# Kernel optimization log

Hardware: AMD Instinct MI355X
Metric: run time of the kernel (lower is better)

## Reference

```python
import jax, jax.numpy as jnp
import numpy as np

VOCAB, EMB, HID, NLAYERS, PAD = 32000, 256, 512, 2, 0


def setup_inputs() -> dict:
    key = jax.random.key(0)
    ks = jax.random.split(key, 20)
    B, T, S = 32, 128, 128
    s = 0.02
    inp = {
        'X': jax.random.randint(ks[0], (B, T), 0, VOCAB, dtype=jnp.int32),
        'encoderOutputs': jax.random.normal(ks[1], (B, S, HID), jnp.float32),
        'hiddeEn': jax.random.normal(ks[2], (2 * NLAYERS, B, HID), jnp.float32),
        'cellEn': jax.random.normal(ks[3], (2 * NLAYERS, B, HID), jnp.float32),
        'emb': jax.random.normal(ks[4], (VOCAB, EMB), jnp.float32) * s,
        'W_ih0': jax.random.normal(ks[5], (4 * HID, EMB), jnp.float32) * s,
        'W_hh0': jax.random.normal(ks[6], (4 * HID, HID), jnp.float32) * s,
        'b_ih0': jnp.zeros((4 * HID,), jnp.float32),
        'b_hh0': jnp.zeros((4 * HID,), jnp.float32),
        'W_ih1': jax.random.normal(ks[7], (4 * HID, HID), jnp.float32) * s,
        'W_hh1': jax.random.normal(ks[8], (4 * HID, HID), jnp.float32) * s,
        'b_ih1': jnp.zeros((4 * HID,), jnp.float32),
        'b_hh1': jnp.zeros((4 * HID,), jnp.float32),
        'attnW': jax.random.normal(ks[9], (HID, 2 * HID), jnp.float32) * s,
        'attnb': jnp.zeros((HID,), jnp.float32),
        'v': jax.random.normal(ks[10], (HID,), jnp.float32) * s,
        'fcW': jax.random.normal(ks[11], (VOCAB, 2 * HID), jnp.float32) * s,
        'fcb': jnp.zeros((VOCAB,), jnp.float32),
    }
    return inp


def _lstm_cell(x, h, c, W_ih, W_hh, b_ih, b_hh):
    gates = x @ W_ih.T + h @ W_hh.T + b_ih + b_hh  # (B, 4H)
    i, f, g, o = jnp.split(gates, 4, axis=-1)  # PyTorch gate order i,f,g,o
    c_new = jax.nn.sigmoid(f) * c + jax.nn.sigmoid(i) * jnp.tanh(g)
    h_new = jax.nn.sigmoid(o) * jnp.tanh(c_new)
    return h_new, c_new


def reference(X, encoderOutputs, hiddeEn, cellEn, emb,
              W_ih0, W_hh0, b_ih0, b_hh0, W_ih1, W_hh1, b_ih1, b_hh1,
              attnW, attnb, v, fcW, fcb):
    B, T = X.shape
    # bridge bidirectional encoder state -> (L, B, H)
    h0 = hiddeEn.reshape(NLAYERS, 2, B, HID).mean(axis=1)
    c0 = cellEn.reshape(NLAYERS, 2, B, HID).mean(axis=1)
    E = emb[X[:, :-1]]            # (B, T-1, EMB)
    targets = X[:, 1:]            # (B, T-1)
    layers = ((W_ih0, W_hh0, b_ih0, b_hh0), (W_ih1, W_hh1, b_ih1, b_hh1))
    enc = encoderOutputs          # (B, S, H)

    def step(carry, xs):
        h, c = carry              # (L, B, H) each
        x_t, y_t = xs             # (B, EMB), (B,)
        x = x_t
        hs, cs = [], []
        for l in range(NLAYERS):
            hn, cn = _lstm_cell(x, h[l], c[l], *layers[l])
            hs.append(hn); cs.append(cn)
            x = hn
        h_new = jnp.stack(hs); c_new = jnp.stack(cs)
        output = x                # (B, H) top-layer output
        hq = h_new[-1]            # attention query
        # additive attention: tanh(W[hq; enc]) . v
        cat = jnp.concatenate([jnp.broadcast_to(hq[:, None, :], enc.shape), enc], axis=-1)
        energy = jnp.tanh(cat @ attnW.T + attnb)           # (B, S, H)
        scores = energy @ v                                 # (B, S)
        att = jax.nn.softmax(scores, axis=1)
        weighted = jnp.einsum('bs,bsh->bh', att, enc)       # (B, H)
        logits = jnp.concatenate([output, weighted], axis=-1) @ fcW.T + fcb  # (B, V)
        logp = jax.nn.log_softmax(logits, axis=-1)
        nll = -jnp.take_along_axis(logp, y_t[:, None], axis=1)[:, 0]
        valid = (y_t != PAD).astype(logits.dtype)
        loss_t = jnp.sum(nll * valid) / jnp.maximum(jnp.sum(valid), 1.0)
        return (h_new, c_new), loss_t

    (_, _), losses = jax.lax.scan(step, (h0, c0),
                                  (E.transpose(1, 0, 2), targets.T))
    return jnp.sum(losses) / (T - 1)
```

## Files before the change

### kernel.cpp

```cpp
#include <hip/hip_runtime.h>
#include <math.h>

#define VOCAB 32000
#define EMB   256
#define HID   512
#define NB    32
#define TT    128
#define TM1   127
#define SS    128
#define NROWS (TM1*NB)
#define NT128 250

#define OFF_ENCW 0
#define OFF_W0S  1048576
#define OFF_W1S  1310720
#define OFF_H0I  1572864
#define OFF_C0I  1589248
#define OFF_H1I  1605632
#define OFF_C1I  1622016
#define OFF_H0H  1638400
#define OFF_HQ   OFF_H0H
#define OFF_GX   2686976
#define OFF_PART OFF_GX
#define OFF_ENCB OFF_GX
#define OFF_CATB 6881280
#define OFF_EMBB OFF_CATB
#define OFF_NLL  8978432
#define OFF_CNT  8982528
#define OFF_CMB0 8986624
#define OFF_CMB1 8988672
#define OFF_WX1  8990720
#define OFF_CMBX 9252864
#define OFF_H08  9254912
#define OFF_FLG  9779200

typedef __attribute__((ext_vector_type(8))) short short8;
typedef __attribute__((ext_vector_type(4))) float f32x4;
typedef unsigned long long ull_t;

__device__ __forceinline__ float sigm(float x){ return 1.f/(1.f + __expf(-x)); }
__device__ __forceinline__ float tanh_f(float x){
    x = fminf(fmaxf(x, -15.f), 15.f);
    float e = __expf(2.f*x);
    return (e-1.f)/(e+1.f);
}
__device__ __forceinline__ unsigned short f2b(float f){
    union{float f; unsigned u;} x{f};
    unsigned r = (x.u + 0x7fff + ((x.u>>16)&1)) >> 16;
    return (unsigned short)r;
}
__device__ __forceinline__ float b2f(unsigned short b){
    union{unsigned u; float f;} x{(unsigned)b<<16};
    return x.f;
}
__device__ __forceinline__ ull_t cohl(const ull_t* p){
    return __hip_atomic_load((ull_t*)p, __ATOMIC_RELAXED, __HIP_MEMORY_SCOPE_AGENT);
}
__device__ __forceinline__ void cohs(ull_t* p, ull_t v){
    __hip_atomic_store(p, v, __ATOMIC_RELAXED, __HIP_MEMORY_SCOPE_AGENT);
}
__device__ __forceinline__ int cohli(const int* p){
    return __hip_atomic_load((int*)p, __ATOMIC_RELAXED, __HIP_MEMORY_SCOPE_AGENT);
}
__device__ __forceinline__ void cohsi(int* p, int v){
    __hip_atomic_store(p, v, __ATOMIC_RELAXED, __HIP_MEMORY_SCOPE_AGENT);
}
__device__ __forceinline__ unsigned short cohls(const unsigned short* p){
    return __hip_atomic_load((unsigned short*)p, __ATOMIC_RELAXED, __HIP_MEMORY_SCOPE_AGENT);
}
__device__ __forceinline__ void cohss(unsigned short* p, unsigned short v){
    __hip_atomic_store(p, v, __ATOMIC_RELAXED, __HIP_MEMORY_SCOPE_AGENT);
}

__global__ void k_init(const float* __restrict__ hid, const float* __restrict__ cel,
                       float* __restrict__ ws){
    int idx = blockIdx.x*256 + threadIdx.x;
    if (idx < 32768){
        int l = idx >> 14, r = idx & 16383;
        int b = r >> 9, k = r & 511;
        float hv = 0.5f*(hid[(2*l)*16384 + b*512 + k] + hid[(2*l+1)*16384 + b*512 + k]);
        float cv = 0.5f*(cel[(2*l)*16384 + b*512 + k] + cel[(2*l+1)*16384 + b*512 + k]);
        ws[(l ? OFF_H1I : OFF_H0I) + b*512 + k] = hv;
        ws[(l ? OFF_C1I : OFF_C0I) + b*512 + k] = cv;
    } else if (idx < 65536){
        int j = idx - 32768;
        ((unsigned short*)(ws + OFF_CATB))[(size_t)4064*1024 + j] = 0;
    } else if (idx < 67584){
        ((int*)(ws + OFF_FLG))[idx - 65536] = 0;
    }
}

__global__ void __launch_bounds__(256)
k_qpack(const float* __restrict__ Whh0, const float* __restrict__ Whh1,
        const float* __restrict__ Wih1, float* __restrict__ ws){
    __shared__ float red[256];
    __shared__ char qb[512];
    const int r = blockIdx.x;
    const int layer = r >> 11, row = r & 2047;
    const int g = row >> 9, u = row & 511;
    const float* W = (layer == 0) ? Whh0 : (layer == 1 ? Whh1 : Wih1);
    const float* src = W + (size_t)row*512;
    const int tid = threadIdx.x;
    float w0 = src[tid], w1 = src[tid+256];
    red[tid] = fmaxf(fabsf(w0), fabsf(w1));
    __syncthreads();
    for (int off = 128; off >= 1; off >>= 1){
        if (tid < off) red[tid] = fmaxf(red[tid], red[tid+off]);
        __syncthreads();
    }
    float mx = fmaxf(red[0], 1e-30f);
    float qs = 127.f / mx;
    qb[tid]     = (char)__float2int_rn(w0*qs);
    qb[tid+256] = (char)__float2int_rn(w1*qs);
    __syncthreads();
    const int woff = (layer == 0) ? OFF_W0S : (layer == 1 ? OFF_W1S : OFF_WX1);
    const int soff = (layer == 0) ? OFF_CMB0 : (layer == 1 ? OFF_CMB1 : OFF_CMBX);
    if (tid < 128){
        int k = tid*4;
        unsigned d =  (unsigned)(unsigned char)qb[k]
                   | ((unsigned)(unsigned char)qb[k+1] << 8)
                   | ((unsigned)(unsigned char)qb[k+2] << 16)
                   | ((unsigned)(unsigned char)qb[k+3] << 24);
        ((unsigned*)(ws + woff))[(((g*32 + (k>>4))*512) + u)*4 + ((k>>2)&3)] = d;
    }
    if (tid == 0) ws[soff + row] = mx / (127.f*127.f);
}

__global__ void k_cvt(const int* __restrict__ X, const float* __restrict__ emb,
                      const float* __restrict__ enc, float* __restrict__ ws){
    int tix = blockIdx.x*256 + threadIdx.x;
    if (tix < 524288){
        int j = tix*4;
        unsigned short* eb = (unsigned short*)(ws + OFF_ENCB);
        #pragma unroll
        for (int e = 0; e < 4; ++e) eb[j+e] = f2b(enc[j+e]);
    } else if (tix < 784480){
        int j = (tix - 524288)*4;
        if (j < NROWS*EMB){
            int m = j >> 8, k = j & 255;
            int b = m / 127, t = m % 127;
            const float* src = emb + (size_t)X[b*TT + t]*EMB + k;
            unsigned short* mb = (unsigned short*)(ws + OFF_EMBB);
            #pragma unroll
            for (int e = 0; e < 4; ++e) mb[(size_t)m*256 + k + e] = f2b(src[e]);
        }
    }
}

#define DOTLOOP(WP, HQARR, A0, A1, A2, A3) \
    _Pragma("unroll 4") \
    for (int kc2 = 0; kc2 < 32; ++kc2){ \
        uint4 hq = *(const uint4*)&HQARR[kc2*16]; \
        uint4 w0 = WP[(0*32 + kc2)*512]; \
        uint4 w1 = WP[(1*32 + kc2)*512]; \
        uint4 w2 = WP[(2*32 + kc2)*512]; \
        uint4 w3 = WP[(3*32 + kc2)*512]; \
        A0 = __builtin_amdgcn_sdot4((int)w0.x, (int)hq.x, A0, false); \
        A0 = __builtin_amdgcn_sdot4((int)w0.y, (int)hq.y, A0, false); \
        A0 = __builtin_amdgcn_sdot4((int)w0.z, (int)hq.z, A0, false); \
        A0 = __builtin_amdgcn_sdot4((int)w0.w, (int)hq.w, A0, false); \
        A1 = __builtin_amdgcn_sdot4((int)w1.x, (int)hq.x, A1, false); \
        A1 = __builtin_amdgcn_sdot4((int)w1.y, (int)hq.y, A1, false); \
        A1 = __builtin_amdgcn_sdot4((int)w1.z, (int)hq.z, A1, false); \
        A1 = __builtin_amdgcn_sdot4((int)w1.w, (int)hq.w, A1, false); \
        A2 = __builtin_amdgcn_sdot4((int)w2.x, (int)hq.x, A2, false); \
        A2 = __builtin_amdgcn_sdot4((int)w2.y, (int)hq.y, A2, false); \
        A2 = __builtin_amdgcn_sdot4((int)w2.z, (int)hq.z, A2, false); \
        A2 = __builtin_amdgcn_sdot4((int)w2.w, (int)hq.w, A2, false); \
        A3 = __builtin_amdgcn_sdot4((int)w3.x, (int)hq.x, A3, false); \
        A3 = __builtin_amdgcn_sdot4((int)w3.y, (int)hq.y, A3, false); \
        A3 = __builtin_amdgcn_sdot4((int)w3.z, (int)hq.z, A3, false); \
        A3 = __builtin_amdgcn_sdot4((int)w3.w, (int)hq.w, A3, false); \
    }

__global__ void __launch_bounds__(512, 1)
k_pipe(const float* __restrict__ bih1, const float* __restrict__ bhh1,
       float* __restrict__ ws)
{
    __shared__ __align__(16) char hh8[512];
    __shared__ float wred[8];
    __shared__ float hfacs;
    const int blk = blockIdx.x, u = threadIdx.x;
    const int role = blk >> 5, b = blk & 31;
    char* h0i8 = (char*)(ws + OFF_H08);
    unsigned short* gx = (unsigned short*)(ws + OFF_GX);
    unsigned short* catb = (unsigned short*)(ws + OFF_CATB);
    int* flag0 = (int*)(ws + OFF_FLG);
    int* flag1 = flag0 + 1024;

    if (role == 0){
        const uint4* wp = ((const uint4*)(ws + OFF_W0S)) + u;
        const float* comb = ws + OFF_CMB0;
        const float cb0 = comb[u], cb1 = comb[512+u], cb2 = comb[1024+u], cb3 = comb[1536+u];
        float c = ws[OFF_C0I + b*512 + u];
        float h0v = ws[OFF_H0I + b*512 + u];
        {
            float a = fabsf(h0v);
            #pragma unroll
            for (int msk = 32; msk >= 1; msk >>= 1) a = fmaxf(a, __shfl_xor(a, msk));
            if ((u & 63) == 0) wred[u >> 6] = a;
            __syncthreads();
            if (u == 0){
                float m = wred[0];
                #pragma unroll
                for (int i2 = 1; i2 < 8; ++i2) m = fmaxf(m, wred[i2]);
                hfacs = fmaxf(m, 1.f);
            }
            __syncthreads();
        }
        float hmaxc = hfacs;
        hh8[u] = (char)__float2int_rn(h0v * (127.f/hmaxc));
        __syncthreads();
        for (int t = 0; t < TM1; ++t){
            const unsigned short* grow = gx + ((size_t)(b*127 + t))*2048 + u;
            float gxi = b2f(grow[0]),    gxf = b2f(grow[512]);
            float gxg = b2f(grow[1024]), gxo = b2f(grow[1536]);
            int a0 = 0, a1 = 0, a2 = 0, a3 = 0;
            DOTLOOP(wp, hh8, a0, a1, a2, a3)
            float gi = fmaf((float)a0, cb0*hmaxc, gxi);
            float gf = fmaf((float)a1, cb1*hmaxc, gxf);
            float gg = fmaf((float)a2, cb2*hmaxc, gxg);
            float go = fmaf((float)a3, cb3*hmaxc, gxo);
            float cn = sigm(gf)*c + sigm(gi)*tanh_f(gg);
            float hn = sigm(go)*tanh_f(cn);
            c = cn;
            __syncthreads();
            hmaxc = 1.f;
            hh8[u] = (char)__float2int_rn(hn * 127.f);
            __syncthreads();
            if (u < 64)
                cohs((ull_t*)(h0i8 + ((size_t)(b*127 + t))*512) + u, ((ull_t*)hh8)[u]);
            __syncthreads();
            if (u == 0) cohsi(flag0 + b*32, t + 1);
        }
    } else if (role == 1){
        __shared__ __align__(16) char h8[512];
        const uint4* wp = ((const uint4*)(ws + OFF_WX1)) + u;
        const float* comb = ws + OFF_CMBX;
        const float cb0 = comb[u], cb1 = comb[512+u], cb2 = comb[1024+u], cb3 = comb[1536+u];
        const float gb0 = bih1[u]        + bhh1[u];
        const float gb1 = bih1[512+u]    + bhh1[512+u];
        const float gb2 = bih1[1024+u]   + bhh1[1024+u];
        const float gb3 = bih1[1536+u]   + bhh1[1536+u];
        for (int t = 0; t < TM1; ++t){
            if (u == 0){
                while (cohli(flag0 + b*32) < t + 1) __builtin_amdgcn_s_sleep(2);
            }
            __syncthreads();
            if (u < 64)
                ((ull_t*)h8)[u] = cohl((const ull_t*)(h0i8 + ((size_t)(b*127 + t))*512) + u);
            __syncthreads();
            int a0 = 0, a1 = 0, a2 = 0, a3 = 0;
            DOTLOOP(wp, h8, a0, a1, a2, a3)
            unsigned short* gr = gx + ((size_t)(b*127 + t))*2048;
            cohss(gr + u,      f2b(fmaf((float)a0, cb0, gb0)));
            cohss(gr + 512+u,  f2b(fmaf((float)a1, cb1, gb1)));
            cohss(gr + 1024+u, f2b(fmaf((float)a2, cb2, gb2)));
            cohss(gr + 1536+u, f2b(fmaf((float)a3, cb3, gb3)));
            __syncthreads();
            if (u == 0) cohsi(flag1 + b*32, t + 1);
        }
    } else {
        const uint4* wp = ((const uint4*)(ws + OFF_W1S)) + u;
        const float* comb = ws + OFF_CMB1;
        const float cb0 = comb[u], cb1 = comb[512+u], cb2 = comb[1024+u], cb3 = comb[1536+u];
        float c = ws[OFF_C1I + b*512 + u];
        float h1v = ws[OFF_H1I + b*512 + u];
        {
            float a = fabsf(h1v);
            #pragma unroll
            for (int msk = 32; msk >= 1; msk >>= 1) a = fmaxf(a, __shfl_xor(a, msk));
            if ((u & 63) == 0) wred[u >> 6] = a;
            __syncthreads();
            if (u == 0){
                float m = wred[0];
                #pragma unroll
                for (int i2 = 1; i2 < 8; ++i2) m = fmaxf(m, wred[i2]);
                hfacs = fmaxf(m, 1.f);
            }
            __syncthreads();
        }
        float hmaxc = hfacs;
        hh8[u] = (char)__float2int_rn(h1v * (127.f/hmaxc));
        __syncthreads();
        for (int t = 0; t < TM1; ++t){
            if (u == 0){
                while (cohli(flag1 + b*32) < t + 1) __builtin_amdgcn_s_sleep(2);
            }
            __syncthreads();
            const unsigned short* gr = gx + ((size_t)(b*127 + t))*2048;
            float gxi = b2f(cohls(gr + u));
            float gxf = b2f(cohls(gr + 512+u));
            float gxg = b2f(cohls(gr + 1024+u));
            float gxo = b2f(cohls(gr + 1536+u));
            int a0 = 0, a1 = 0, a2 = 0, a3 = 0;
            DOTLOOP(wp, hh8, a0, a1, a2, a3)
            float gi = fmaf((float)a0, cb0*hmaxc, gxi);
            float gf = fmaf((float)a1, cb1*hmaxc, gxf);
            float gg = fmaf((float)a2, cb2*hmaxc, gxg);
            float go = fmaf((float)a3, cb3*hmaxc, gxo);
            float cn = sigm(gf)*c + sigm(gi)*tanh_f(gg);
            float hn = sigm(go)*tanh_f(cn);
            c = cn;
            __syncthreads();
            hmaxc = 1.f;
            hh8[u] = (char)__float2int_rn(hn * 127.f);
            catb[((size_t)(t*32 + b))*1024 + u] = f2b(hn);
            __syncthreads();
        }
    }
}

__global__ void __launch_bounds__(256)
k_gemm(const unsigned short* __restrict__ A, int lda,
       const float* __restrict__ B, int ldb,
       const float* __restrict__ bias1, const float* __restrict__ bias2,
       unsigned short* __restrict__ C, int ldc, int nkk)
{
    __shared__ unsigned short As[128*32];
    __shared__ unsigned short Bs[128*32];
    const int tid = threadIdx.x;
    const int mt = blockIdx.x, nt = blockIdx.y;
    const int m0 = mt*128, n0 = nt*128;
    const int lane = tid & 63, wid = tid >> 6;
    const int wr = wid >> 1, wc = wid & 1;
    const int lr = lane & 15, lg = lane >> 4;
    const int ar = tid & 127, ah = tid >> 7;
    const int br = tid >> 1,  bh = tid & 1;
    f32x4 acc[4][4];
    #pragma unroll
    for (int i=0;i<4;i++)
        #pragma unroll
        for (int j=0;j<4;j++) acc[i][j] = (f32x4){0.f,0.f,0.f,0.f};

    for (int kk = 0; kk < nkk; ++kk){
        const int k0 = kk*32;
        uint4 a0 = *(const uint4*)(A + (size_t)(m0+ar)*lda + k0 + ah*16);
        uint4 a1 = *(const uint4*)(A + (size_t)(m0+ar)*lda + k0 + ah*16 + 8);
        const float* bsrc = B + (size_t)(n0+br)*ldb + k0 + bh*16;
        float4 f0 = *(const float4*)(bsrc);
        float4 f1 = *(const float4*)(bsrc+4);
        float4 f2 = *(const float4*)(bsrc+8);
        float4 f3 = *(const float4*)(bsrc+12);
        __syncthreads();
        {
            int swz = (ar>>1)&3;
            *(uint4*)&As[ar*32 + ((2*ah  )^swz)*8] = a0;
            *(uint4*)&As[ar*32 + ((2*ah+1)^swz)*8] = a1;
        }
        {
            uint4 p0, p1;
            p0.x = __builtin_amdgcn_perm(__float_as_uint(f0.y), __float_as_uint(f0.x), 0x07060302u);
            p0.y = __builtin_amdgcn_perm(__float_as_uint(f0.w), __float_as_uint(f0.z), 0x07060302u);
            p0.z = __builtin_amdgcn_perm(__float_as_uint(f1.y), __float_as_uint(f1.x), 0x07060302u);
            p0.w = __builtin_amdgcn_perm(__float_as_uint(f1.w), __float_as_uint(f1.z), 0x07060302u);
            p1.x = __builtin_amdgcn_perm(__float_as_uint(f2.y), __float_as_uint(f2.x), 0x07060302u);
            p1.y = __builtin_amdgcn_perm(__float_as_uint(f2.w), __float_as_uint(f2.z), 0x07060302u);
            p1.z = __builtin_amdgcn_perm(__float_as_uint(f3.y), __float_as_uint(f3.x), 0x07060302u);
            p1.w = __builtin_amdgcn_perm(__float_as_uint(f3.w), __float_as_uint(f3.z), 0x07060302u);
            int swz = (br>>1)&3;
            *(uint4*)&Bs[br*32 + ((2*bh  )^swz)*8] = p0;
            *(uint4*)&Bs[br*32 + ((2*bh+1)^swz)*8] = p1;
        }
        __syncthreads();
        short8 av[4], bv[4];
        #pragma unroll
        for (int mi=0; mi<4; ++mi){
            int r = wr*64 + mi*16 + lr;
            av[mi] = *(const short8*)&As[r*32 + ((lg ^ ((r>>1)&3))*8)];
        }
        #pragma unroll
        for (int ni=0; ni<4; ++ni){
            int r = wc*64 + ni*16 + lr;
            bv[ni] = *(const short8*)&Bs[r*32 + ((lg ^ ((r>>1)&3))*8)];
        }
        #pragma unroll
        for (int mi=0; mi<4; ++mi)
            #pragma unroll
            for (int ni=0; ni<4; ++ni)
                acc[mi][ni] = __builtin_amdgcn_mfma_f32_16x16x32_bf16(av[mi], bv[ni], acc[mi][ni], 0, 0, 0);
    }
    int coln[4]; float bsv[4];
    #pragma unroll
    for (int ni=0; ni<4; ++ni){
        coln[ni] = n0 + wc*64 + ni*16 + lr;
        float bv2 = 0.f;
        if (bias1) bv2 += bias1[coln[ni]];
        if (bias2) bv2 += bias2[coln[ni]];
        bsv[ni] = bv2;
    }
    #pragma unroll
    for (int mi=0; mi<4; ++mi)
        #pragma unroll
        for (int ni=0; ni<4; ++ni)
            #pragma unroll
            for (int reg=0; reg<4; ++reg){
                int row = m0 + wr*64 + mi*16 + lg*4 + reg;
                C[(size_t)row*ldc + coln[ni]] = f2b(acc[mi][ni][reg] + bsv[ni]);
            }
}

__global__ void __launch_bounds__(256)
k_att(const float* __restrict__ enc, const float* __restrict__ v, float* __restrict__ ws){
    __shared__ float hqs[512], vv[512], att[128], rbuf[2];
    const int m = blockIdx.x, tid = threadIdx.x;
    const int b = m & 31;
    const unsigned short* hq = (const unsigned short*)(ws + OFF_HQ) + (size_t)m*512;
    const unsigned short* encwb = (const unsigned short*)(ws + OFF_ENCW);
    unsigned short* catb = (unsigned short*)(ws + OFF_CATB);
    hqs[tid] = b2f(hq[tid]); hqs[tid+256] = b2f(hq[tid+256]);
    vv[tid] = v[tid];        vv[tid+256] = v[tid+256];
    __syncthreads();
    {
        int s = tid >> 1, q = tid & 1;
        const unsigned short* eb = encwb + ((size_t)(b*SS + s))*512 + q*256;
        const float* hp = hqs + q*256;
        const float* vp = vv + q*256;
        float p0 = 0.f, p1 = 0.f;
        #pragma unroll 2
        for (int k = 0; k < 256; k += 2){
            p0 += tanh_f(hp[k]   + b2f(eb[k]))   * vp[k];
            p1 += tanh_f(hp[k+1] + b2f(eb[k+1])) * vp[k+1];
        }
        float p = p0 + p1;
        p += __shfl_xor(p, 1);
        if (q == 0) att[s] = p;
    }
    __syncthreads();
    float e0 = 0.f, e1 = 0.f;
    if (tid < 64){
        float m2 = fmaxf(att[tid], att[tid+64]);
        #pragma unroll
        for (int msk = 32; msk >= 1; msk >>= 1) m2 = fmaxf(m2, __shfl_xor(m2, msk));
        if (tid == 0) rbuf[0] = m2;
    }
    __syncthreads();
    float M = rbuf[0];
    if (tid < 64){
        e0 = __expf(att[tid] - M);
        e1 = __expf(att[tid+64] - M);
        float sum = e0 + e1;
        #pragma unroll
        for (int msk = 32; msk >= 1; msk >>= 1) sum += __shfl_xor(sum, msk);
        if (tid == 0) rbuf[1] = sum;
    }
    __syncthreads();
    if (tid < 64){
        float inv = 1.f / rbuf[1];
        att[tid] = e0*inv; att[tid+64] = e1*inv;
    }
    __syncthreads();
    {
        const float* eb2 = enc + (size_t)(b*SS)*512;
        float w0 = 0.f, w1 = 0.f;
        #pragma unroll 4
        for (int s = 0; s < 128; ++s){
            float a = att[s];
            w0 += a * eb2[s*512 + tid];
            w1 += a * eb2[s*512 + tid + 256];
        }
        catb[((size_t)m)*1024 + 512 + tid] = f2b(w0);
        catb[((size_t)m)*1024 + 768 + tid] = f2b(w1);
    }
}

__global__ void __launch_bounds__(256)
k_fc(const float* __restrict__ fcW, const float* __restrict__ fcb, float* __restrict__ ws){
    __shared__ unsigned short As[128*32];
    __shared__ unsigned short Bs[128*32];
    __shared__ float eM[128], eS[128];
    const int tid = threadIdx.x;
    const int bid = blockIdx.x;
    const int g = (bid & 7)*1000 + (bid >> 3);
    const int nt = g / 32, mt = g % 32;
    const int m0 = mt*128, n0 = nt*128;
    const unsigned short* catb = (const unsigned short*)(ws + OFF_CATB);
    const int lane = tid & 63, wid = tid >> 6;
    const int wr = wid >> 1, wc = wid & 1;
    const int lr = lane & 15, lg = lane >> 4;
    const int ar = tid & 127, ah = tid >> 7;
    const int br = tid >> 1,  bh = tid & 1;
    f32x4 acc[4][4];
    #pragma unroll
    for (int i=0;i<4;i++)
        #pragma unroll
        for (int j=0;j<4;j++) acc[i][j] = (f32x4){0.f,0.f,0.f,0.f};

    for (int kk = 0; kk < 32; ++kk){
        const int k0 = kk*32;
        uint4 a0 = *(const uint4*)(catb + (size_t)(m0+ar)*1024 + k0 + ah*16);
        uint4 a1 = *(const uint4*)(catb + (size_t)(m0+ar)*1024 + k0 + ah*16 + 8);
        const float* bsrc = fcW + (size_t)(n0+br)*1024 + k0 + bh*16;
        float4 f0 = *(const float4*)(bsrc);
        float4 f1 = *(const float4*)(bsrc+4);
        float4 f2 = *(const float4*)(bsrc+8);
        float4 f3 = *(const float4*)(bsrc+12);
        __syncthreads();
        {
            int swz = (ar>>1)&3;
            *(uint4*)&As[ar*32 + ((2*ah  )^swz)*8] = a0;
            *(uint4*)&As[ar*32 + ((2*ah+1)^swz)*8] = a1;
        }
        {
            uint4 p0, p1;
            p0.x = __builtin_amdgcn_perm(__float_as_uint(f0.y), __float_as_uint(f0.x), 0x07060302u);
            p0.y = __builtin_amdgcn_perm(__float_as_uint(f0.w), __float_as_uint(f0.z), 0x07060302u);
            p0.z = __builtin_amdgcn_perm(__float_as_uint(f1.y), __float_as_uint(f1.x), 0x07060302u);
            p0.w = __builtin_amdgcn_perm(__float_as_uint(f1.w), __float_as_uint(f1.z), 0x07060302u);
            p1.x = __builtin_amdgcn_perm(__float_as_uint(f2.y), __float_as_uint(f2.x), 0x07060302u);
            p1.y = __builtin_amdgcn_perm(__float_as_uint(f2.w), __float_as_uint(f2.z), 0x07060302u);
            p1.z = __builtin_amdgcn_perm(__float_as_uint(f3.y), __float_as_uint(f3.x), 0x07060302u);
            p1.w = __builtin_amdgcn_perm(__float_as_uint(f3.w), __float_as_uint(f3.z), 0x07060302u);
            int swz = (br>>1)&3;
            *(uint4*)&Bs[br*32 + ((2*bh  )^swz)*8] = p0;
            *(uint4*)&Bs[br*32 + ((2*bh+1)^swz)*8] = p1;
        }
        __syncthreads();
        short8 av[4], bv[4];
        #pragma unroll
        for (int mi=0; mi<4; ++mi){
            int r = wr*64 + mi*16 + lr;
            av[mi] = *(const short8*)&As[r*32 + ((lg ^ ((r>>1)&3))*8)];
        }
        #pragma unroll
        for (int ni=0; ni<4; ++ni){
            int r = wc*64 + ni*16 + lr;
            bv[ni] = *(const short8*)&Bs[r*32 + ((lg ^ ((r>>1)&3))*8)];
        }
        #pragma unroll
        for (int mi=0; mi<4; ++mi)
            #pragma unroll
            for (int ni=0; ni<4; ++ni)
                acc[mi][ni] = __builtin_amdgcn_mfma_f32_16x16x32_bf16(av[mi], bv[ni], acc[mi][ni], 0, 0, 0);
    }
    float bias[4];
    #pragma unroll
    for (int ni=0; ni<4; ++ni) bias[ni] = fcb[n0 + wc*64 + ni*16 + lr];
    float mxA[4][4], smA[4][4];
    #pragma unroll
    for (int mi=0; mi<4; ++mi){
        #pragma unroll
        for (int reg=0; reg<4; ++reg){
            float mx = -3.4e38f;
            #pragma unroll
            for (int ni=0; ni<4; ++ni) mx = fmaxf(mx, acc[mi][ni][reg] + bias[ni]);
            #pragma unroll
            for (int msk=8; msk>=1; msk>>=1) mx = fmaxf(mx, __shfl_xor(mx, msk));
            float sm = 0.f;
            #pragma unroll
            for (int ni=0; ni<4; ++ni) sm += __expf(acc[mi][ni][reg] + bias[ni] - mx);
            #pragma unroll
            for (int msk=8; msk>=1; msk>>=1) sm += __shfl_xor(sm, msk);
            mxA[mi][reg] = mx; smA[mi][reg] = sm;
            if (wc == 0 && lr == 0){
                int rl = wr*64 + mi*16 + lg*4 + reg;
                eM[rl] = mx; eS[rl] = sm;
            }
        }
    }
    __syncthreads();
    if (wc == 1 && lr == 0){
        float2* part = (float2*)(ws + OFF_PART);
        #pragma unroll
        for (int mi=0; mi<4; ++mi){
            #pragma unroll
            for (int reg=0; reg<4; ++reg){
                int rl = wr*64 + mi*16 + lg*4 + reg;
                float m0v = eM[rl], s0 = eS[rl];
                float m1v = mxA[mi][reg], s1 = smA[mi][reg];
                float M = fmaxf(m0v, m1v);
                float S = s0*__expf(m0v - M) + s1*__expf(m1v - M);
                part[(size_t)(m0 + rl)*NT128 + nt] = make_float2(M, S);
            }
        }
    }
}

__global__ void k_row(const int* __restrict__ X, const float* __restrict__ fcW,
                      const float* __restrict__ fcb, float* __restrict__ ws){
    __shared__ float LM[256], LS[256];
    int m = blockIdx.x, tid = threadIdx.x;
    const float2* p = (const float2*)(ws + OFF_PART);
    float M = -3.4e38f, Ssum = 0.f;
    if (tid < NT128){
        float2 q = p[(size_t)m*NT128 + tid];
        M = q.x; Ssum = q.y;
    }
    LM[tid] = M; LS[tid] = Ssum;
    __syncthreads();
    for (int off = 128; off >= 1; off >>= 1){
        if (tid < off){
            float m1 = LM[tid], s1 = LS[tid];
            float m2 = LM[tid+off], s2 = LS[tid+off];
            float mm = fmaxf(m1, m2);
            LM[tid] = mm;
            LS[tid] = s1*__expf(m1-mm) + s2*__expf(m2-mm);
        }
        __syncthreads();
    }
    float lse = LM[0] + __logf(LS[0]);
    __syncthreads();
    int t = m >> 5, b = m & 31;
    int y = X[b*TT + t + 1];
    const unsigned short* cr = (const unsigned short*)(ws + OFF_CATB) + (size_t)m*1024;
    const float* wr = fcW + (size_t)y*1024;
    float a = 0.f;
    #pragma unroll
    for (int k = 0; k < 4; ++k) a += b2f(cr[tid*4+k]) * wr[tid*4+k];
    LM[tid] = a;
    __syncthreads();
    for (int off = 128; off >= 1; off >>= 1){
        if (tid < off) LM[tid] += LM[tid+off];
        __syncthreads();
    }
    if (tid == 0){
        float tl = LM[0] + fcb[y];
        float nll = lse - tl;
        int valid = (y != 0);
        ws[OFF_NLL + m] = valid ? nll : 0.f;
        ws[OFF_CNT + m] = valid ? 1.f : 0.f;
    }
}

__global__ void k_fin(const float* __restrict__ ws, float* __restrict__ out){
    __shared__ float red[256];
    int tid = threadIdx.x;
    float lt = 0.f;
    if (tid < TM1){
        float s = 0.f, c = 0.f;
        for (int b=0;b<NB;b++){
            s += ws[OFF_NLL + tid*NB + b];
            c += ws[OFF_CNT + tid*NB + b];
        }
        lt = s / fmaxf(c, 1.f);
    }
    red[tid] = lt;
    __syncthreads();
    for (int off=128; off>=1; off>>=1){
        if (tid < off) red[tid] += red[tid+off];
        __syncthreads();
    }
    if (tid == 0) out[0] = red[0] / (float)TM1;
}

extern "C" void kernel_launch(void* const* d_in, const int* in_sizes, int n_in,
                              void* d_out, int out_size, void* d_ws, size_t ws_size,
                              hipStream_t stream) {
    const int*   X     = (const int*)  d_in[0];
    const float* enc   = (const float*)d_in[1];
    const float* hid   = (const float*)d_in[2];
    const float* cel   = (const float*)d_in[3];
    const float* emb   = (const float*)d_in[4];
    const float* Wih0  = (const float*)d_in[5];
    const float* Whh0  = (const float*)d_in[6];
    const float* bih0  = (const float*)d_in[7];
    const float* bhh0  = (const float*)d_in[8];
    const float* Wih1  = (const float*)d_in[9];
    const float* Whh1  = (const float*)d_in[10];
    const float* bih1  = (const float*)d_in[11];
    const float* bhh1  = (const float*)d_in[12];
    const float* attnW = (const float*)d_in[13];
    const float* attnb = (const float*)d_in[14];
    const float* v     = (const float*)d_in[15];
    const float* fcW   = (const float*)d_in[16];
    const float* fcb   = (const float*)d_in[17];
    float* ws  = (float*)d_ws;
    float* out = (float*)d_out;

    unsigned short* catb = (unsigned short*)(ws + OFF_CATB);
    unsigned short* hq   = (unsigned short*)(ws + OFF_HQ);
    unsigned short* encb = (unsigned short*)(ws + OFF_ENCB);
    unsigned short* embb = (unsigned short*)(ws + OFF_EMBB);
    unsigned short* encw = (unsigned short*)(ws + OFF_ENCW);
    unsigned short* g0x  = (unsigned short*)(ws + OFF_GX);

    k_init<<<320, 256, 0, stream>>>(hid, cel, ws);
    k_qpack<<<6144, 256, 0, stream>>>(Whh0, Whh1, Wih1, ws);
    k_cvt<<<3065, 256, 0, stream>>>(X, emb, enc, ws);
    k_gemm<<<dim3(32,4), 256, 0, stream>>>(encb, 512, attnW + 512, 1024,
                                           attnb, (const float*)nullptr,
                                           encw, 512, 16);
    k_gemm<<<dim3(32,16), 256, 0, stream>>>(embb, 256, Wih0, 256, bih0, bhh0,
                                            g0x, 2048, 8);
    {
        void* args[] = {(void*)&bih1, (void*)&bhh1, (void*)&ws};
        (void)hipLaunchCooperativeKernel((const void*)k_pipe, dim3(96), dim3(512),
                                         args, 0, stream);
    }
    k_gemm<<<dim3(32,4), 256, 0, stream>>>(catb, 1024, attnW, 1024,
                                           (const float*)nullptr, (const float*)nullptr,
                                           hq, 512, 16);
    k_att<<<NROWS, 256, 0, stream>>>(enc, v, ws);
    k_fc<<<8000, 256, 0, stream>>>(fcW, fcb, ws);
    k_row<<<NROWS, 256, 0, stream>>>(X, fcW, fcb, ws);
    k_fin<<<1, 256, 0, stream>>>(ws, out);
}
```

Measured before the change: 2.077 ms.

## Fuse attention into the persistent LSTM pipeline as a fourth role of blocks

Adds a fourth group of 32 blocks to the cooperative pipeline kernel. Each block waits on a per-step flag from layer 1, computes the query projection with an int8-quantized attnW via sdot4, then the additive attention scores, the softmax and the weighted context, and writes them into the concat buffer. This removes the separate query GEMM and attention kernel launches and overlaps attention with the recurrence. It adds int8 quantization error on the query projection, along with per-step sequential work that could lengthen the pipeline's critical path if the attention role lags behind the LSTM roles.

```diff
diff --git a/kernel.cpp b/kernel.cpp
--- a/kernel.cpp
+++ b/kernel.cpp
@@ -18,8 +18,6 @@
 #define OFF_C0I  1589248
 #define OFF_H1I  1605632
 #define OFF_C1I  1622016
-#define OFF_H0H  1638400
-#define OFF_HQ   OFF_H0H
 #define OFF_GX   2686976
 #define OFF_PART OFF_GX
 #define OFF_ENCB OFF_GX
@@ -33,6 +31,9 @@
 #define OFF_CMBX 9252864
 #define OFF_H08  9254912
 #define OFF_FLG  9779200
+#define OFF_WQ8  9782272
+#define OFF_CMQ  9847808
+#define OFF_H18  9848320
 
 typedef __attribute__((ext_vector_type(8))) short short8;
 typedef __attribute__((ext_vector_type(4))) float f32x4;
@@ -85,21 +86,25 @@
     } else if (idx < 65536){
         int j = idx - 32768;
         ((unsigned short*)(ws + OFF_CATB))[(size_t)4064*1024 + j] = 0;
-    } else if (idx < 67584){
+    } else if (idx < 68608){
         ((int*)(ws + OFF_FLG))[idx - 65536] = 0;
     }
 }
 
 __global__ void __launch_bounds__(256)
 k_qpack(const float* __restrict__ Whh0, const float* __restrict__ Whh1,
-        const float* __restrict__ Wih1, float* __restrict__ ws){
+        const float* __restrict__ Wih1, const float* __restrict__ attnW,
+        float* __restrict__ ws){
     __shared__ float red[256];
     __shared__ char qb[512];
     const int r = blockIdx.x;
     const int layer = r >> 11, row = r & 2047;
     const int g = row >> 9, u = row & 511;
-    const float* W = (layer == 0) ? Whh0 : (layer == 1 ? Whh1 : Wih1);
-    const float* src = W + (size_t)row*512;
+    const float* src;
+    if (layer == 0)      src = Whh0 + (size_t)row*512;
+    else if (layer == 1) src = Whh1 + (size_t)row*512;
+    else if (layer == 2) src = Wih1 + (size_t)row*512;
+    else                 src = attnW + (size_t)row*1024;
     const int tid = threadIdx.x;
     float w0 = src[tid], w1 = src[tid+256];
     red[tid] = fmaxf(fabsf(w0), fabsf(w1));
@@ -113,8 +118,10 @@
     qb[tid]     = (char)__float2int_rn(w0*qs);
     qb[tid+256] = (char)__float2int_rn(w1*qs);
     __syncthreads();
-    const int woff = (layer == 0) ? OFF_W0S : (layer == 1 ? OFF_W1S : OFF_WX1);
-    const int soff = (layer == 0) ? OFF_CMB0 : (layer == 1 ? OFF_CMB1 : OFF_CMBX);
+    const int woff = (layer == 0) ? OFF_W0S : (layer == 1 ? OFF_W1S :
+                     (layer == 2 ? OFF_WX1 : OFF_WQ8));
+    const int soff = (layer == 0) ? OFF_CMB0 : (layer == 1 ? OFF_CMB1 :
+                     (layer == 2 ? OFF_CMBX : OFF_CMQ));
     if (tid < 128){
         int k = tid*4;
         unsigned d =  (unsigned)(unsigned char)qb[k]
@@ -175,6 +182,7 @@
 
 __global__ void __launch_bounds__(512, 1)
 k_pipe(const float* __restrict__ bih1, const float* __restrict__ bhh1,
+       const float* __restrict__ enc, const float* __restrict__ v,
        float* __restrict__ ws)
 {
     __shared__ __align__(16) char hh8[512];
@@ -183,10 +191,12 @@
     const int blk = blockIdx.x, u = threadIdx.x;
     const int role = blk >> 5, b = blk & 31;
     char* h0i8 = (char*)(ws + OFF_H08);
+    char* h1i8 = (char*)(ws + OFF_H18);
     unsigned short* gx = (unsigned short*)(ws + OFF_GX);
     unsigned short* catb = (unsigned short*)(ws + OFF_CATB);
     int* flag0 = (int*)(ws + OFF_FLG);
     int* flag1 = flag0 + 1024;
+    int* flag2 = flag0 + 2048;
 
     if (role == 0){
         const uint4* wp = ((const uint4*)(ws + OFF_W0S)) + u;
@@ -260,7 +270,7 @@
             __syncthreads();
             if (u == 0) cohsi(flag1 + b*32, t + 1);
         }
-    } else {
+    } else if (role == 2){
         const uint4* wp = ((const uint4*)(ws + OFF_W1S)) + u;
         const float* comb = ws + OFF_CMB1;
         const float cb0 = comb[u], cb1 = comb[512+u], cb2 = comb[1024+u], cb3 = comb[1536+u];
@@ -306,6 +316,92 @@
             hmaxc = 1.f;
             hh8[u] = (char)__float2int_rn(hn * 127.f);
             catb[((size_t)(t*32 + b))*1024 + u] = f2b(hn);
+            __syncthreads();
+            if (u < 64)
+                cohs((ull_t*)(h1i8 + ((size_t)(b*127 + t))*512) + u, ((ull_t*)hh8)[u]);
+            __syncthreads();
+            if (u == 0) cohsi(flag2 + b*32, t + 1);
+        }
+    } else {
+        __shared__ __align__(16) char h1q[512];
+        __shared__ float hqf[512], vvv[512], attv[128], rbuf[2];
+        const uint4* wq = (const uint4*)(ws + OFF_WQ8);
+        const float scq = ws[OFF_CMQ + u];
+        const unsigned short* encwb = (const unsigned short*)(ws + OFF_ENCW);
+        vvv[u] = v[u];
+        __syncthreads();
+        for (int t = 0; t < TM1; ++t){
+            if (u == 0){
+                while (cohli(flag2 + b*32) < t + 1) __builtin_amdgcn_s_sleep(2);
+            }
+            __syncthreads();
+            if (u < 64)
+                ((ull_t*)h1q)[u] = cohl((const ull_t*)(h1i8 + ((size_t)(b*127 + t))*512) + u);
+            __syncthreads();
+            {
+                int a = 0;
+                #pragma unroll 4
+                for (int kc2 = 0; kc2 < 32; ++kc2){
+                    uint4 hv = *(const uint4*)&h1q[kc2*16];
+                    uint4 w = wq[kc2*512 + u];
+                    a = __builtin_amdgcn_sdot4((int)w.x, (int)hv.x, a, false);
+                    a = __builtin_amdgcn_sdot4((int)w.y, (int)hv.y, a, false);
+                    a = __builtin_amdgcn_sdot4((int)w.z, (int)hv.z, a, false);
+                    a = __builtin_amdgcn_sdot4((int)w.w, (int)hv.w, a, false);
+                }
+                hqf[u] = (float)a * scq;
+            }
+            __syncthreads();
+            {
+                int s = u >> 2, q = u & 3;
+                const unsigned short* eb = encwb + ((size_t)(b*SS + s))*512 + q*128;
+                const float* hp = hqf + q*128;
+                const float* vp = vvv + q*128;
+                float p0 = 0.f, p1 = 0.f;
+                #pragma unroll 2
+                for (int k = 0; k < 128; k += 2){
+                    p0 += tanh_f(hp[k]   + b2f(eb[k]))   * vp[k];
+                    p1 += tanh_f(hp[k+1] + b2f(eb[k+1])) * vp[k+1];
+                }
+                float p = p0 + p1;
+                p += __shfl_xor(p, 1);
+                p += __shfl_xor(p, 2);
+                if (q == 0) attv[s] = p;
+            }
+            __syncthreads();
+            float e0 = 0.f, e1 = 0.f;
+            if (u < 64){
+                float m2 = fmaxf(attv[u], attv[u+64]);
+                #pragma unroll
+                for (int msk = 32; msk >= 1; msk >>= 1) m2 = fmaxf(m2, __shfl_xor(m2, msk));
+                if (u == 0) rbuf[0] = m2;
+            }
+            __syncthreads();
+            float M = rbuf[0];
+            if (u < 64){
+                e0 = __expf(attv[u] - M);
+                e1 = __expf(attv[u+64] - M);
+                float sum = e0 + e1;
+                #pragma unroll
+                for (int msk = 32; msk >= 1; msk >>= 1) sum += __shfl_xor(sum, msk);
+                if (u == 0) rbuf[1] = sum;
+            }
+            __syncthreads();
+            if (u < 64){
+                float inv = 1.f / rbuf[1];
+                attv[u] = e0*inv; attv[u+64] = e1*inv;
+            }
+            __syncthreads();
+            {
+                const float* eb2 = enc + ((size_t)(b*SS))*512 + u;
+                float w0 = 0.f, w1 = 0.f;
+                #pragma unroll 4
+                for (int s = 0; s < 128; s += 2){
+                    w0 += attv[s]   * eb2[(s  )*512];
+                    w1 += attv[s+1] * eb2[(s+1)*512];
+                }
+                catb[((size_t)(t*32 + b))*1024 + 512 + u] = f2b(w0 + w1);
+            }
             __syncthreads();
         }
     }
@@ -398,70 +494,6 @@
                 int row = m0 + wr*64 + mi*16 + lg*4 + reg;
                 C[(size_t)row*ldc + coln[ni]] = f2b(acc[mi][ni][reg] + bsv[ni]);
             }
-}
-
-__global__ void __launch_bounds__(256)
-k_att(const float* __restrict__ enc, const float* __restrict__ v, float* __restrict__ ws){
-    __shared__ float hqs[512], vv[512], att[128], rbuf[2];
-    const int m = blockIdx.x, tid = threadIdx.x;
-    const int b = m & 31;
-    const unsigned short* hq = (const unsigned short*)(ws + OFF_HQ) + (size_t)m*512;
-    const unsigned short* encwb = (const unsigned short*)(ws + OFF_ENCW);
-    unsigned short* catb = (unsigned short*)(ws + OFF_CATB);
-    hqs[tid] = b2f(hq[tid]); hqs[tid+256] = b2f(hq[tid+256]);
-    vv[tid] = v[tid];        vv[tid+256] = v[tid+256];
-    __syncthreads();
-    {
-        int s = tid >> 1, q = tid & 1;
-        const unsigned short* eb = encwb + ((size_t)(b*SS + s))*512 + q*256;
-        const float* hp = hqs + q*256;
-        const float* vp = vv + q*256;
-        float p0 = 0.f, p1 = 0.f;
-        #pragma unroll 2
-        for (int k = 0; k < 256; k += 2){
-            p0 += tanh_f(hp[k]   + b2f(eb[k]))   * vp[k];
-            p1 += tanh_f(hp[k+1] + b2f(eb[k+1])) * vp[k+1];
-        }
-        float p = p0 + p1;
-        p += __shfl_xor(p, 1);
-        if (q == 0) att[s] = p;
-    }
-    __syncthreads();
-    float e0 = 0.f, e1 = 0.f;
-    if (tid < 64){
-        float m2 = fmaxf(att[tid], att[tid+64]);
-        #pragma unroll
-        for (int msk = 32; msk >= 1; msk >>= 1) m2 = fmaxf(m2, __shfl_xor(m2, msk));
-        if (tid == 0) rbuf[0] = m2;
-    }
-    __syncthreads();
-    float M = rbuf[0];
-    if (tid < 64){
-        e0 = __expf(att[tid] - M);
-        e1 = __expf(att[tid+64] - M);
-        float sum = e0 + e1;
-        #pragma unroll
-        for (int msk = 32; msk >= 1; msk >>= 1) sum += __shfl_xor(sum, msk);
-        if (tid == 0) rbuf[1] = sum;
-    }
-    __syncthreads();
-    if (tid < 64){
-        float inv = 1.f / rbuf[1];
-        att[tid] = e0*inv; att[tid+64] = e1*inv;
-    }
-    __syncthreads();
-    {
-        const float* eb2 = enc + (size_t)(b*SS)*512;
-        float w0 = 0.f, w1 = 0.f;
-        #pragma unroll 4
-        for (int s = 0; s < 128; ++s){
-            float a = att[s];
-            w0 += a * eb2[s*512 + tid];
-            w1 += a * eb2[s*512 + tid + 256];
-        }
-        catb[((size_t)m)*1024 + 512 + tid] = f2b(w0);
-        catb[((size_t)m)*1024 + 768 + tid] = f2b(w1);
-    }
 }
 
 __global__ void __launch_bounds__(256)
@@ -667,15 +699,13 @@
     float* ws  = (float*)d_ws;
     float* out = (float*)d_out;
 
-    unsigned short* catb = (unsigned short*)(ws + OFF_CATB);
-    unsigned short* hq   = (unsigned short*)(ws + OFF_HQ);
     unsigned short* encb = (unsigned short*)(ws + OFF_ENCB);
     unsigned short* embb = (unsigned short*)(ws + OFF_EMBB);
     unsigned short* encw = (unsigned short*)(ws + OFF_ENCW);
     unsigned short* g0x  = (unsigned short*)(ws + OFF_GX);
 
     k_init<<<320, 256, 0, stream>>>(hid, cel, ws);
-    k_qpack<<<6144, 256, 0, stream>>>(Whh0, Whh1, Wih1, ws);
+    k_qpack<<<6656, 256, 0, stream>>>(Whh0, Whh1, Wih1, attnW, ws);
     k_cvt<<<3065, 256, 0, stream>>>(X, emb, enc, ws);
     k_gemm<<<dim3(32,4), 256, 0, stream>>>(encb, 512, attnW + 512, 1024,
                                            attnb, (const float*)nullptr,
@@ -683,14 +713,10 @@
     k_gemm<<<dim3(32,16), 256, 0, stream>>>(embb, 256, Wih0, 256, bih0, bhh0,
                                             g0x, 2048, 8);
     {
-        void* args[] = {(void*)&bih1, (void*)&bhh1, (void*)&ws};
-        (void)hipLaunchCooperativeKernel((const void*)k_pipe, dim3(96), dim3(512),
+        void* args[] = {(void*)&bih1, (void*)&bhh1, (void*)&enc, (void*)&v, (void*)&ws};
+        (void)hipLaunchCooperativeKernel((const void*)k_pipe, dim3(128), dim3(512),
                                          args, 0, stream);
     }
-    k_gemm<<<dim3(32,4), 256, 0, stream>>>(catb, 1024, attnW, 1024,
-                                           (const float*)nullptr, (const float*)nullptr,
-                                           hq, 512, 16);
-    k_att<<<NROWS, 256, 0, stream>>>(enc, v, ws);
     k_fc<<<8000, 256, 0, stream>>>(fcW, fcb, ws);
     k_row<<<NROWS, 256, 0, stream>>>(X, fcW, fcb, ws);
     k_fin<<<1, 256, 0, stream>>>(ws, out);
```

Result: slower. 3.132 ms (+50.8%).
